# Kernel optimization log

Hardware: AMD Instinct MI355X
Metric: run time of the kernel (lower is better)

Reference implementation:

```python
import jax, jax.numpy as jnp
import numpy as np

B, LQ, LK = 4, 512, 512
QF, KF, H, VD = 256, 256, 128, 256


def setup_inputs() -> dict:
    key = jax.random.key(0)
    ks = jax.random.split(key, 7)
    queries = jax.random.normal(ks[0], (B, LQ, QF), dtype=jnp.float32)
    keys = jax.random.normal(ks[1], (B, LK, KF), dtype=jnp.float32)
    values = jax.random.normal(ks[2], (B, LK, VD), dtype=jnp.float32)
    valid_lens = jax.random.randint(ks[3], (B,), 1, LK + 1)  # at least 1 valid key
    # nn.Linear weights (torch layout: [out_features, in_features]), Kaiming-uniform-ish scale
    W_q = jax.random.normal(ks[4], (H, QF), dtype=jnp.float32) / np.sqrt(QF).astype(np.float32)
    W_k = jax.random.normal(ks[5], (H, KF), dtype=jnp.float32) / np.sqrt(KF).astype(np.float32)
    W_v = jax.random.normal(ks[6], (H,), dtype=jnp.float32) / np.sqrt(H).astype(np.float32)
    return {"queries": queries, "keys": keys, "values": values,
            "valid_lens": valid_lens, "W_q": W_q, "W_k": W_k, "W_v": W_v}


def reference(queries, keys, values, valid_lens, W_q, W_k, W_v):
    # Projections: a(q,k) = W_v^T tanh(W_q q + W_k k)
    q = jnp.einsum('bqf,hf->bqh', queries, W_q)   # [B,LQ,H]
    k = jnp.einsum('bkf,hf->bkh', keys, W_k)      # [B,LK,H]
    feats = jnp.tanh(q[:, :, None, :] + k[:, None, :, :])  # [B,LQ,LK,H]
    scores = jnp.einsum('bqkh,h->bqk', feats, W_v)          # [B,LQ,LK]
    # masked softmax over key axis: positions >= valid_len get -1e9
    key_pos = jnp.arange(scores.shape[-1])[None, None, :]   # [1,1,LK]
    mask = key_pos < valid_lens[:, None, None]               # [B,1,LK] broadcasts over LQ
    scores = jnp.where(mask, scores, jnp.float32(-1e9))
    attn = jax.nn.softmax(scores, axis=-1)                   # [B,LQ,LK]
    # dropout p=0.0 (eval) -> identity
    out = jnp.einsum('bqk,bkv->bqv', attn, values)           # [B,LQ,VD]
    return out, attn
```

## Files before the change

kernel.cpp:

```cpp
#include <hip/hip_runtime.h>
#include <cstddef>

#define NB 4
#define LQ 512
#define LK 512
#define QF 256
#define NH 128
#define VD 256

__device__ __forceinline__ float fexp2(float x) {
    float r; asm("v_exp_f32 %0, %1" : "=v"(r) : "v"(x)); return r;
}
__device__ __forceinline__ float frcp(float x) {
    float r; asm("v_rcp_f32 %0, %1" : "=v"(r) : "v"(x)); return r;
}

constexpr float kLog2e    = 1.4426950408889634f;
constexpr float kPreScale = 2.0f * kLog2e;

constexpr int TI = 16;

__global__ __launch_bounds__(256) void proj_kernel(
    const float* __restrict__ queries, const float* __restrict__ keys,
    const float* __restrict__ W_q, const float* __restrict__ W_k,
    float* __restrict__ eq, float* __restrict__ ekt)
{
    const int id    = blockIdx.x;
    const int which = id & 1;
    const int rt    = (id >> 1) & 127;
    const int ht    = id >> 8;
    const float* In = which ? keys : queries;
    const float* W  = which ? W_k  : W_q;
    const int row0  = rt * TI;

    __shared__ float rows[TI][QF + 4];

    const int t = threadIdx.x;
    {
        const int f4 = t & 63;
        const int tr = t >> 6;
        const float4* In4 = (const float4*)In;
        #pragma unroll
        for (int k = 0; k < TI / 4; ++k) {
            const int r = tr + 4 * k;
            ((float4*)&rows[r][0])[f4] = In4[(size_t)(row0 + r) * 64 + f4];
        }
    }
    __syncthreads();

    const int i0 = t & 3;
    const int h  = ht * 64 + (t >> 2);
    float acc[4] = {0.f, 0.f, 0.f, 0.f};

    const float4* W4 = (const float4*)(W + (size_t)h * QF);
    #pragma unroll 4
    for (int f4 = 0; f4 < QF / 4; ++f4) {
        const float4 w = W4[f4];
        #pragma unroll
        for (int r = 0; r < 4; ++r) {
            const float4 x = *(const float4*)&rows[i0 + 4 * r][f4 * 4];
            acc[r] += w.x * x.x + w.y * x.y + w.z * x.z + w.w * x.w;
        }
    }

    if (which == 0) {
        #pragma unroll
        for (int r = 0; r < 4; ++r)
            eq[(size_t)(row0 + i0 + 4 * r) * NH + h] = fexp2(kPreScale * acc[r]);
    } else {
        #pragma unroll
        for (int r = 0; r < 4; ++r) {
            const int row = row0 + i0 + 4 * r;
            const int b   = row >> 9;
            const int rl  = row & 511;
            ekt[((size_t)b * NH + h) * LK + rl] = fexp2(kPreScale * acc[r]);
        }
    }
}

__global__ __launch_bounds__(256, 8) void score_kernel(
    const float* __restrict__ eq, const float* __restrict__ ekt,
    const int* __restrict__ valid_lens, const float* __restrict__ W_v,
    float* __restrict__ scores)
{
    const int id  = blockIdx.x;
    const int it  = id & 63;
    const int bjc = id >> 6;
    const int b   = bjc >> 3;
    const int jc  = bjc & 7;
    const int vl  = valid_lens[b];
    if (jc * 64 >= vl) return;

    __shared__ float q_lds[8][NH];
    __shared__ float wv[NH];

    const int t  = threadIdx.x;
    const int i0 = it * 8;
    #pragma unroll
    for (int r = 0; r < 4; ++r)
        ((float*)q_lds)[t + 256 * r] = eq[(size_t)(b * LQ + i0) * NH + t + 256 * r];
    if (t < NH) wv[t] = W_v[t];
    __syncthreads();

    const int wid  = t >> 6;
    const int lane = t & 63;
    const float4* qa4 = (const float4*)q_lds[2 * wid];
    const float4* qb4 = (const float4*)q_lds[2 * wid + 1];
    const float4* wv4 = (const float4*)wv;

    float sumW = 0.f;
    #pragma unroll 8
    for (int h4 = 0; h4 < NH / 4; ++h4) {
        const float4 w = wv4[h4];
        sumW += (w.x + w.y) + (w.z + w.w);
    }

    const float* p = ekt + (size_t)b * NH * LK + jc * 64 + lane;
    float aA0 = 0.f, aA1 = 0.f, aA2 = 0.f, aA3 = 0.f;
    float aB0 = 0.f, aB1 = 0.f, aB2 = 0.f, aB3 = 0.f;
    #pragma unroll 4
    for (int h4 = 0; h4 < NH / 4; ++h4) {
        const float e0 = p[(size_t)(4 * h4 + 0) * LK];
        const float e1 = p[(size_t)(4 * h4 + 1) * LK];
        const float e2 = p[(size_t)(4 * h4 + 2) * LK];
        const float e3 = p[(size_t)(4 * h4 + 3) * LK];
        const float4 w  = wv4[h4];
        const float4 qa = qa4[h4];
        const float4 qb = qb4[h4];
        aA0 = __builtin_fmaf(w.x, frcp(__builtin_fmaf(qa.x, e0, 1.f)), aA0);
        aA1 = __builtin_fmaf(w.y, frcp(__builtin_fmaf(qa.y, e1, 1.f)), aA1);
        aA2 = __builtin_fmaf(w.z, frcp(__builtin_fmaf(qa.z, e2, 1.f)), aA2);
        aA3 = __builtin_fmaf(w.w, frcp(__builtin_fmaf(qa.w, e3, 1.f)), aA3);
        aB0 = __builtin_fmaf(w.x, frcp(__builtin_fmaf(qb.x, e0, 1.f)), aB0);
        aB1 = __builtin_fmaf(w.y, frcp(__builtin_fmaf(qb.y, e1, 1.f)), aB1);
        aB2 = __builtin_fmaf(w.z, frcp(__builtin_fmaf(qb.z, e2, 1.f)), aB2);
        aB3 = __builtin_fmaf(w.w, frcp(__builtin_fmaf(qb.w, e3, 1.f)), aB3);
    }
    const float sA = __builtin_fmaf(-2.f, (aA0 + aA1) + (aA2 + aA3), sumW);
    const float sB = __builtin_fmaf(-2.f, (aB0 + aB1) + (aB2 + aB3), sumW);

    const int ra = i0 + 2 * wid;
    scores[((size_t)b * LQ + ra)     * LK + jc * 64 + lane] = sA;
    scores[((size_t)b * LQ + ra + 1) * LK + jc * 64 + lane] = sB;
}

constexpr int TQ = 4;

__global__ __launch_bounds__(1024, 8) void smpv_kernel(
    const float* __restrict__ values, const int* __restrict__ valid_lens,
    float* __restrict__ out, float* __restrict__ attn_out )
{
    const int blk = blockIdx.x;
    const int b   = blk >> 7;
    const int i0  = (blk & 127) * TQ;

    __shared__ float attn_lds[TQ][LK];
    __shared__ float pacc[TQ][TQ][VD];
    __shared__ float redm[16];
    __shared__ float reds[16];

    const int t    = threadIdx.x;
    const int wid  = t >> 6;
    const int lane = t & 63;
    const int qi   = wid & 3;
    const int g    = wid >> 2;
    const int i    = i0 + qi;
    const int vl   = valid_lens[b];

    const float* srow = attn_out + (size_t)(b * LQ + i) * LK;
    float s[2];
    #pragma unroll
    for (int u = 0; u < 2; ++u) {
        const int jj = g + 4 * u;
        s[u] = 0.f;
        if (jj * 64 < vl) s[u] = srow[jj * 64 + lane];
    }

    float m = -1e30f;
    #pragma unroll
    for (int u = 0; u < 2; ++u) {
        const int j = lane + 64 * (g + 4 * u);
        if (j < vl) m = fmaxf(m, s[u]);
    }
    #pragma unroll
    for (int off = 1; off < 64; off <<= 1)
        m = fmaxf(m, __shfl_xor(m, off, 64));
    if (lane == 0) redm[wid] = m;
    __syncthreads();
    m = fmaxf(fmaxf(redm[qi], redm[qi + 4]), fmaxf(redm[qi + 8], redm[qi + 12]));

    float p[2];
    float sum = 0.f;
    #pragma unroll
    for (int u = 0; u < 2; ++u) {
        const int j = lane + 64 * (g + 4 * u);
        const float e = (j < vl) ? fexp2((s[u] - m) * kLog2e) : 0.f;
        p[u] = e;
        sum += e;
    }
    #pragma unroll
    for (int off = 1; off < 64; off <<= 1)
        sum += __shfl_xor(sum, off, 64);
    if (lane == 0) reds[wid] = sum;
    __syncthreads();
    const float rs = frcp((reds[qi] + reds[qi + 4]) + (reds[qi + 8] + reds[qi + 12]));

    float* attn_row = attn_out + (size_t)(b * LQ + i) * LK;
    #pragma unroll
    for (int u = 0; u < 2; ++u) {
        const int j = lane + 64 * (g + 4 * u);
        const float a = p[u] * rs;
        attn_lds[qi][j] = a;
        attn_row[j]     = a;
    }
    __syncthreads();

    const int g2  = t >> 8;
    const int c   = t & 255;
    const int vlr = (vl + 3) & ~3;
    const int j0  = g2 * 128;
    const int j1  = min(j0 + 128, vlr);

    float acc[TQ] = {0.f, 0.f, 0.f, 0.f};
    const float* vcol = values + (size_t)b * LK * VD + c;
    for (int j = j0; j < j1; j += 4) {
        const float v0 = vcol[(size_t)(j + 0) * VD];
        const float v1 = vcol[(size_t)(j + 1) * VD];
        const float v2 = vcol[(size_t)(j + 2) * VD];
        const float v3 = vcol[(size_t)(j + 3) * VD];
        #pragma unroll
        for (int ii = 0; ii < TQ; ++ii) {
            const float4 a = *(const float4*)&attn_lds[ii][j];
            acc[ii] += a.x * v0 + a.y * v1 + a.z * v2 + a.w * v3;
        }
    }
    #pragma unroll
    for (int ii = 0; ii < TQ; ++ii) pacc[g2][ii][c] = acc[ii];
    __syncthreads();

    {
        const int ii = t >> 8;
        const int cc = t & 255;
        out[(size_t)(b * LQ + i0 + ii) * VD + cc] =
            (pacc[0][ii][cc] + pacc[1][ii][cc]) + (pacc[2][ii][cc] + pacc[3][ii][cc]);
    }
}

extern "C" void kernel_launch(void* const* d_in, const int* in_sizes, int n_in,
                              void* d_out, int out_size, void* d_ws, size_t ws_size,
                              hipStream_t stream)
{
    const float* queries    = (const float*)d_in[0];
    const float* keys       = (const float*)d_in[1];
    const float* values     = (const float*)d_in[2];
    const int*   valid_lens = (const int*)  d_in[3];
    const float* W_q        = (const float*)d_in[4];
    const float* W_k        = (const float*)d_in[5];
    const float* W_v        = (const float*)d_in[6];

    float* out      = (float*)d_out;
    float* attn_out = out + (size_t)NB * LQ * VD;

    float* eq  = (float*)d_ws;
    float* ekt = eq + (size_t)NB * LQ * NH;

    proj_kernel <<<512, 256, 0, stream>>>(queries, keys, W_q, W_k, eq, ekt);
    score_kernel<<<2048, 256, 0, stream>>>(eq, ekt, valid_lens, W_v, attn_out);
    smpv_kernel <<<NB * (LQ / TQ), 1024, 0, stream>>>(values, valid_lens, out, attn_out);
}
```

Before: 40.96 us.

## Use static softmax bound, pre-transpose weights, and retile projection and PV kernels

The score kernel now writes exp(score - sum|W_v|) directly, using sum|W_v| as a fixed upper bound on the score. This removes the max-reduction pass from the softmax kernel, which then only normalizes. A new kernel transposes W_q/W_k so projection threads read coalesced weights, the projection processes 8 rows per thread, and the key output goes through an LDS transpose for coalesced stores. The PV kernel now handles 8 queries per block with float4 value loads, at the cost of an extra launch and some risk of underflow in exp for strongly negative scores.

```diff
diff --git a/kernel.cpp b/kernel.cpp
--- a/kernel.cpp
+++ b/kernel.cpp
@@ -14,66 +14,85 @@
 __device__ __forceinline__ float frcp(float x) {
     float r; asm("v_rcp_f32 %0, %1" : "=v"(r) : "v"(x)); return r;
 }
+__device__ __forceinline__ void fma4(float4& acc, float s, const float4 v) {
+    acc.x = __builtin_fmaf(s, v.x, acc.x);
+    acc.y = __builtin_fmaf(s, v.y, acc.y);
+    acc.z = __builtin_fmaf(s, v.z, acc.z);
+    acc.w = __builtin_fmaf(s, v.w, acc.w);
+}
 
 constexpr float kLog2e    = 1.4426950408889634f;
 constexpr float kPreScale = 2.0f * kLog2e;
 
-constexpr int TI = 16;
+__global__ __launch_bounds__(256) void transw_kernel(
+    const float* __restrict__ W_q, const float* __restrict__ W_k,
+    float4* __restrict__ wt)
+{
+    const int bid = blockIdx.x;
+    const int mat = bid & 1;
+    const int f4b = (bid >> 1) * 8;
+    const float4* W4 = (const float4*)(mat ? W_k : W_q);
+    float4* o = wt + (size_t)mat * 64 * NH;
+
+    const int t  = threadIdx.x;
+    const int h  = t & 127;
+    const int fo = t >> 7;
+    #pragma unroll
+    for (int it = 0; it < 4; ++it) {
+        const int f4 = f4b + fo + 2 * it;
+        o[f4 * NH + h] = W4[h * 64 + f4];
+    }
+}
 
 __global__ __launch_bounds__(256) void proj_kernel(
     const float* __restrict__ queries, const float* __restrict__ keys,
-    const float* __restrict__ W_q, const float* __restrict__ W_k,
+    const float4* __restrict__ wt,
     float* __restrict__ eq, float* __restrict__ ekt)
 {
-    const int id    = blockIdx.x;
-    const int which = id & 1;
-    const int rt    = (id >> 1) & 127;
-    const int ht    = id >> 8;
-    const float* In = which ? keys : queries;
-    const float* W  = which ? W_k  : W_q;
-    const int row0  = rt * TI;
-
-    __shared__ float rows[TI][QF + 4];
-
-    const int t = threadIdx.x;
-    {
-        const int f4 = t & 63;
-        const int tr = t >> 6;
-        const float4* In4 = (const float4*)In;
-        #pragma unroll
-        for (int k = 0; k < TI / 4; ++k) {
-            const int r = tr + 4 * k;
-            ((float4*)&rows[r][0])[f4] = In4[(size_t)(row0 + r) * 64 + f4];
-        }
-    }
-    __syncthreads();
-
-    const int i0 = t & 3;
-    const int h  = ht * 64 + (t >> 2);
-    float acc[4] = {0.f, 0.f, 0.f, 0.f};
-
-    const float4* W4 = (const float4*)(W + (size_t)h * QF);
+    const int bid   = blockIdx.x;
+    const int which = bid & 1;
+    const int rt    = bid >> 1;
+    const int row0  = rt * 16;
+    const float4* In4 = (const float4*)(which ? keys : queries);
+    const float4* w4  = wt + (size_t)which * 64 * NH;
+
+    __shared__ float et[16][NH + 1];
+
+    const int t    = threadIdx.x;
+    const int lane = t & 63;
+    const int wid  = t >> 6;
+    const int h    = (wid & 1) * 64 + lane;
+    const int rb   = __builtin_amdgcn_readfirstlane((wid >> 1) * 8);
+
+    float acc[8] = {0.f, 0.f, 0.f, 0.f, 0.f, 0.f, 0.f, 0.f};
+    const float4* Inb = In4 + (size_t)(row0 + rb) * 64;
     #pragma unroll 4
-    for (int f4 = 0; f4 < QF / 4; ++f4) {
-        const float4 w = W4[f4];
-        #pragma unroll
-        for (int r = 0; r < 4; ++r) {
-            const float4 x = *(const float4*)&rows[i0 + 4 * r][f4 * 4];
-            acc[r] += w.x * x.x + w.y * x.y + w.z * x.z + w.w * x.w;
+    for (int f4 = 0; f4 < 64; ++f4) {
+        const float4 w = w4[f4 * NH + h];
+        #pragma unroll
+        for (int k = 0; k < 8; ++k) {
+            const float4 x = Inb[(size_t)k * 64 + f4];
+            acc[k] += w.x * x.x + w.y * x.y + w.z * x.z + w.w * x.w;
         }
     }
 
     if (which == 0) {
         #pragma unroll
-        for (int r = 0; r < 4; ++r)
-            eq[(size_t)(row0 + i0 + 4 * r) * NH + h] = fexp2(kPreScale * acc[r]);
+        for (int k = 0; k < 8; ++k)
+            eq[(size_t)(row0 + rb + k) * NH + h] = fexp2(kPreScale * acc[k]);
     } else {
         #pragma unroll
-        for (int r = 0; r < 4; ++r) {
-            const int row = row0 + i0 + 4 * r;
-            const int b   = row >> 9;
-            const int rl  = row & 511;
-            ekt[((size_t)b * NH + h) * LK + rl] = fexp2(kPreScale * acc[r]);
+        for (int k = 0; k < 8; ++k)
+            et[rb + k][h] = fexp2(kPreScale * acc[k]);
+        __syncthreads();
+        const int rl = t & 15;
+        const int h0 = t >> 4;
+        const int b  = row0 >> 9;
+        const int j0 = row0 & 511;
+        #pragma unroll
+        for (int pass = 0; pass < 8; ++pass) {
+            const int hh = h0 + 16 * pass;
+            ekt[((size_t)b * NH + hh) * LK + j0 + rl] = et[rl][hh];
         }
     }
 }
@@ -81,7 +100,7 @@
 __global__ __launch_bounds__(256, 8) void score_kernel(
     const float* __restrict__ eq, const float* __restrict__ ekt,
     const int* __restrict__ valid_lens, const float* __restrict__ W_v,
-    float* __restrict__ scores)
+    float* __restrict__ pout)
 {
     const int id  = blockIdx.x;
     const int it  = id & 63;
@@ -108,22 +127,23 @@
     const float4* qb4 = (const float4*)q_lds[2 * wid + 1];
     const float4* wv4 = (const float4*)wv;
 
-    float sumW = 0.f;
+    float sumW = 0.f, sumA = 0.f;
     #pragma unroll 8
     for (int h4 = 0; h4 < NH / 4; ++h4) {
         const float4 w = wv4[h4];
         sumW += (w.x + w.y) + (w.z + w.w);
-    }
-
-    const float* p = ekt + (size_t)b * NH * LK + jc * 64 + lane;
+        sumA += (fabsf(w.x) + fabsf(w.y)) + (fabsf(w.z) + fabsf(w.w));
+    }
+
+    const float* pk = ekt + (size_t)b * NH * LK + jc * 64 + lane;
     float aA0 = 0.f, aA1 = 0.f, aA2 = 0.f, aA3 = 0.f;
     float aB0 = 0.f, aB1 = 0.f, aB2 = 0.f, aB3 = 0.f;
     #pragma unroll 4
     for (int h4 = 0; h4 < NH / 4; ++h4) {
-        const float e0 = p[(size_t)(4 * h4 + 0) * LK];
-        const float e1 = p[(size_t)(4 * h4 + 1) * LK];
-        const float e2 = p[(size_t)(4 * h4 + 2) * LK];
-        const float e3 = p[(size_t)(4 * h4 + 3) * LK];
+        const float e0 = pk[(size_t)(4 * h4 + 0) * LK];
+        const float e1 = pk[(size_t)(4 * h4 + 1) * LK];
+        const float e2 = pk[(size_t)(4 * h4 + 2) * LK];
+        const float e3 = pk[(size_t)(4 * h4 + 3) * LK];
         const float4 w  = wv4[h4];
         const float4 qa = qa4[h4];
         const float4 qb = qb4[h4];
@@ -138,63 +158,46 @@
     }
     const float sA = __builtin_fmaf(-2.f, (aA0 + aA1) + (aA2 + aA3), sumW);
     const float sB = __builtin_fmaf(-2.f, (aB0 + aB1) + (aB2 + aB3), sumW);
+    const float pA = fexp2((sA - sumA) * kLog2e);
+    const float pB = fexp2((sB - sumA) * kLog2e);
 
     const int ra = i0 + 2 * wid;
-    scores[((size_t)b * LQ + ra)     * LK + jc * 64 + lane] = sA;
-    scores[((size_t)b * LQ + ra + 1) * LK + jc * 64 + lane] = sB;
-}
-
-constexpr int TQ = 4;
-
-__global__ __launch_bounds__(1024, 8) void smpv_kernel(
+    pout[((size_t)b * LQ + ra)     * LK + jc * 64 + lane] = pA;
+    pout[((size_t)b * LQ + ra + 1) * LK + jc * 64 + lane] = pB;
+}
+
+__global__ __launch_bounds__(1024) void normpv_kernel(
     const float* __restrict__ values, const int* __restrict__ valid_lens,
     float* __restrict__ out, float* __restrict__ attn_out )
 {
     const int blk = blockIdx.x;
-    const int b   = blk >> 7;
-    const int i0  = (blk & 127) * TQ;
-
-    __shared__ float attn_lds[TQ][LK];
-    __shared__ float pacc[TQ][TQ][VD];
-    __shared__ float redm[16];
-    __shared__ float reds[16];
+    const int b   = blk >> 6;
+    const int i0  = (blk & 63) * 8;
+
+    __shared__ float  attn_t[LK][12];
+    __shared__ float4 pacc[8][8][VD / 4];
+    __shared__ float  reds[16];
 
     const int t    = threadIdx.x;
     const int wid  = t >> 6;
     const int lane = t & 63;
-    const int qi   = wid & 3;
-    const int g    = wid >> 2;
-    const int i    = i0 + qi;
     const int vl   = valid_lens[b];
 
-    const float* srow = attn_out + (size_t)(b * LQ + i) * LK;
-    float s[2];
-    #pragma unroll
-    for (int u = 0; u < 2; ++u) {
-        const int jj = g + 4 * u;
-        s[u] = 0.f;
-        if (jj * 64 < vl) s[u] = srow[jj * 64 + lane];
-    }
-
-    float m = -1e30f;
-    #pragma unroll
-    for (int u = 0; u < 2; ++u) {
-        const int j = lane + 64 * (g + 4 * u);
-        if (j < vl) m = fmaxf(m, s[u]);
-    }
-    #pragma unroll
-    for (int off = 1; off < 64; off <<= 1)
-        m = fmaxf(m, __shfl_xor(m, off, 64));
-    if (lane == 0) redm[wid] = m;
-    __syncthreads();
-    m = fmaxf(fmaxf(redm[qi], redm[qi + 4]), fmaxf(redm[qi + 8], redm[qi + 12]));
-
-    float p[2];
+    const int qi = wid & 7;
+    const int g  = wid >> 3;
+    float* arow = attn_out + (size_t)(b * LQ + i0 + qi) * LK;
+
+    float p[4];
     float sum = 0.f;
     #pragma unroll
-    for (int u = 0; u < 2; ++u) {
-        const int j = lane + 64 * (g + 4 * u);
-        const float e = (j < vl) ? fexp2((s[u] - m) * kLog2e) : 0.f;
+    for (int u = 0; u < 4; ++u) {
+        const int jj = g + 2 * u;
+        const int j  = jj * 64 + lane;
+        float e = 0.f;
+        if (jj * 64 < vl) {
+            e = arow[j];
+            if (j >= vl) e = 0.f;
+        }
         p[u] = e;
         sum += e;
     }
@@ -203,46 +206,63 @@
         sum += __shfl_xor(sum, off, 64);
     if (lane == 0) reds[wid] = sum;
     __syncthreads();
-    const float rs = frcp((reds[qi] + reds[qi + 4]) + (reds[qi + 8] + reds[qi + 12]));
-
-    float* attn_row = attn_out + (size_t)(b * LQ + i) * LK;
-    #pragma unroll
-    for (int u = 0; u < 2; ++u) {
-        const int j = lane + 64 * (g + 4 * u);
+    const float rs = frcp(reds[qi] + reds[qi + 8]);
+
+    #pragma unroll
+    for (int u = 0; u < 4; ++u) {
+        const int j = (g + 2 * u) * 64 + lane;
         const float a = p[u] * rs;
-        attn_lds[qi][j] = a;
-        attn_row[j]     = a;
-    }
-    __syncthreads();
-
-    const int g2  = t >> 8;
-    const int c   = t & 255;
-    const int vlr = (vl + 3) & ~3;
-    const int j0  = g2 * 128;
-    const int j1  = min(j0 + 128, vlr);
-
-    float acc[TQ] = {0.f, 0.f, 0.f, 0.f};
-    const float* vcol = values + (size_t)b * LK * VD + c;
-    for (int j = j0; j < j1; j += 4) {
-        const float v0 = vcol[(size_t)(j + 0) * VD];
-        const float v1 = vcol[(size_t)(j + 1) * VD];
-        const float v2 = vcol[(size_t)(j + 2) * VD];
-        const float v3 = vcol[(size_t)(j + 3) * VD];
-        #pragma unroll
-        for (int ii = 0; ii < TQ; ++ii) {
-            const float4 a = *(const float4*)&attn_lds[ii][j];
-            acc[ii] += a.x * v0 + a.y * v1 + a.z * v2 + a.w * v3;
-        }
-    }
-    #pragma unroll
-    for (int ii = 0; ii < TQ; ++ii) pacc[g2][ii][c] = acc[ii];
+        arow[j]       = a;
+        attn_t[j][qi] = a;
+    }
+    __syncthreads();
+
+    const int j0 = wid * 32;
+    const int j1 = min(j0 + 32, vl);
+    float4 acc4[8];
+    #pragma unroll
+    for (int q = 0; q < 8; ++q) acc4[q] = float4{0.f, 0.f, 0.f, 0.f};
+
+    const float4* v4 = (const float4*)(values + (size_t)b * LK * VD);
+    for (int j = j0; j < j1; ++j) {
+        const float4 a0 = *(const float4*)&attn_t[j][0];
+        const float4 a1 = *(const float4*)&attn_t[j][4];
+        const float4 vv = v4[(size_t)j * 64 + lane];
+        fma4(acc4[0], a0.x, vv); fma4(acc4[1], a0.y, vv);
+        fma4(acc4[2], a0.z, vv); fma4(acc4[3], a0.w, vv);
+        fma4(acc4[4], a1.x, vv); fma4(acc4[5], a1.y, vv);
+        fma4(acc4[6], a1.z, vv); fma4(acc4[7], a1.w, vv);
+    }
+
+    if (wid < 8) {
+        #pragma unroll
+        for (int q = 0; q < 8; ++q) pacc[wid][q][lane] = acc4[q];
+    }
+    __syncthreads();
+    if (wid >= 8) {
+        #pragma unroll
+        for (int q = 0; q < 8; ++q) {
+            const float4 pv = pacc[wid - 8][q][lane];
+            pacc[wid - 8][q][lane] =
+                float4{pv.x + acc4[q].x, pv.y + acc4[q].y,
+                       pv.z + acc4[q].z, pv.w + acc4[q].w};
+        }
+    }
     __syncthreads();
 
     {
-        const int ii = t >> 8;
-        const int cc = t & 255;
-        out[(size_t)(b * LQ + i0 + ii) * VD + cc] =
-            (pacc[0][ii][cc] + pacc[1][ii][cc]) + (pacc[2][ii][cc] + pacc[3][ii][cc]);
+        const int q = t >> 7;
+        const int c = t & 127;
+        float s0 = 0.f, s1 = 0.f;
+        #pragma unroll
+        for (int k = 0; k < 8; ++k) {
+            const float* pf = (const float*)&pacc[k][q][0];
+            s0 += pf[c];
+            s1 += pf[c + 128];
+        }
+        float* orow = out + (size_t)(b * LQ + i0 + q) * VD;
+        orow[c]       = s0;
+        orow[c + 128] = s1;
     }
 }
 
@@ -261,10 +281,12 @@
     float* out      = (float*)d_out;
     float* attn_out = out + (size_t)NB * LQ * VD;
 
-    float* eq  = (float*)d_ws;
-    float* ekt = eq + (size_t)NB * LQ * NH;
-
-    proj_kernel <<<512, 256, 0, stream>>>(queries, keys, W_q, W_k, eq, ekt);
-    score_kernel<<<2048, 256, 0, stream>>>(eq, ekt, valid_lens, W_v, attn_out);
-    smpv_kernel <<<NB * (LQ / TQ), 1024, 0, stream>>>(values, valid_lens, out, attn_out);
-}
+    float*  eq  = (float*)d_ws;
+    float*  ekt = eq + (size_t)NB * LQ * NH;
+    float4* wt  = (float4*)(ekt + (size_t)NB * NH * LK);
+
+    transw_kernel<<<16,   256, 0, stream>>>(W_q, W_k, wt);
+    proj_kernel  <<<256,  256, 0, stream>>>(queries, keys, wt, eq, ekt);
+    score_kernel <<<2048, 256, 0, stream>>>(eq, ekt, valid_lens, W_v, attn_out);
+    normpv_kernel<<<256, 1024, 0, stream>>>(values, valid_lens, out, attn_out);
+}
```

Measured after the change: 50.32 us. 22.8% more time.
